# Optimization experiments

Hardware: AMD Instinct MI355X
Metric: run time of the kernel (lower is better)

The kernel has to match this reference:

```python
import jax, jax.numpy as jnp
from jax import lax
import numpy as np

B, CIN, COUT, H, W = 32, 64, 64, 128, 128
KH = KW = 1
STRIDE = (1, 1)
PADDING = ((0, 0), (0, 0))


def setup_inputs() -> dict:
    key = jax.random.key(0)
    k1, k2, k3, k4 = jax.random.split(key, 4)
    x_quant = jax.random.randint(k1, (B, CIN, H, W), 0, 256, dtype=jnp.int32)  # uint8 values
    weight_int8 = jax.random.randint(k2, (COUT, CIN, KH, KW), -127, 128, dtype=jnp.int32)
    weight_scale = jax.random.uniform(k3, (COUT, 1, 1, 1), dtype=jnp.float32, minval=0.001, maxval=0.02)
    weight_zero_point = jnp.zeros((COUT, 1, 1, 1), dtype=jnp.int32)
    bias_fp32 = jax.random.normal(k4, (COUT,), dtype=jnp.float32) * 0.1
    return {
        "x_quant": x_quant,
        "input_scale": jnp.float32(0.02),
        "input_zero_point": jnp.int32(128),
        "weight_int8": weight_int8,
        "weight_scale": weight_scale,
        "weight_zero_point": weight_zero_point,
        "bias_fp32": bias_fp32,
        "output_scale": jnp.float32(0.05),
        "output_zero_point": jnp.int32(128),
    }


def reference(x_quant, input_scale, input_zero_point, weight_int8, weight_scale,
              weight_zero_point, bias_fp32, output_scale, output_zero_point):
    # dequant (zero-point subtract) in fp32
    x = x_quant.astype(jnp.float32) - input_zero_point.astype(jnp.float32)          # [B,Cin,H,W]
    w = weight_int8.astype(jnp.float32) - weight_zero_point.astype(jnp.float32)     # [O,I,kh,kw]
    conv = lax.conv_general_dilated(
        x, w, window_strides=STRIDE, padding=PADDING,
        dimension_numbers=("NCHW", "OIHW", "NCHW"))                                 # [B,O,H',W']
    # requantize: per-out-channel scale + bias, round, clamp to uint8 range
    requant_scale = (input_scale * weight_scale / output_scale).reshape(1, COUT, 1, 1)
    bias_term = (bias_fp32 / output_scale).reshape(1, COUT, 1, 1)
    final_float = conv * requant_scale + bias_term
    requant = jnp.round(final_float) + output_zero_point.astype(jnp.float32)
    out_q = jnp.clip(requant, 0.0, 255.0).astype(jnp.uint8)
    return out_q
```

## Files before the change

### kernel.cpp

```cpp
#include <hip/hip_runtime.h>

#define CIN   64
#define COUT  64
#define HW    16384
#define NPIX  (32 * HW)

#define BLOCKS 512
#define SPAN   1024
#define GRP    128
#define NGRP   (SPAN / GRP)

__global__ void prep_kernel(const int* __restrict__ w,
                            const float* __restrict__ wscale,
                            const int* __restrict__ wzp,
                            const float* __restrict__ bias,
                            const float* __restrict__ is_p,
                            const int* __restrict__ izp_p,
                            const float* __restrict__ os_p,
                            const int* __restrict__ ozp_p,
                            int* __restrict__ wp,
                            float4* __restrict__ params) {
    int o = threadIdx.x;
    if (o >= COUT) return;
    int zp = wzp[o];
    int sum = 0;
    #pragma unroll
    for (int k = 0; k < 16; ++k) {
        int c0 = w[o * CIN + 4 * k + 0] - zp;
        int c1 = w[o * CIN + 4 * k + 1] - zp;
        int c2 = w[o * CIN + 4 * k + 2] - zp;
        int c3 = w[o * CIN + 4 * k + 3] - zp;
        sum += c0 + c1 + c2 + c3;
        wp[o * 16 + k] = (c0 & 0xff) | ((c1 & 0xff) << 8) |
                         ((c2 & 0xff) << 16) | ((c3 & 0xff) << 24);
    }
    float4 pr;
    pr.x = is_p[0] * wscale[o] / os_p[0];
    pr.y = bias[o] / os_p[0] + (float)ozp_p[0];
    pr.z = 0.0f;
    pr.w = __int_as_float((128 - izp_p[0]) * sum);
    params[o] = pr;
}

__global__ __launch_bounds__(256) void conv_kernel(
    const int* __restrict__ x,
    const int* __restrict__ wp_g,
    const float4* __restrict__ params_g,
    int* __restrict__ out) {

    __shared__ int s_x[2][CIN * GRP];

    const int tid  = threadIdx.x;
    const int lane = tid & 63;
    const int wv   = tid >> 6;
    const int px   = tid & (GRP - 1);
    const int oh   = __builtin_amdgcn_readfirstlane(tid >> 7);

    const int pix_base = blockIdx.x * SPAN;
    const int bimg = pix_base >> 14;
    const int p0   = pix_base & (HW - 1);
    const int* ximg = x   + bimg * (CIN * HW) + p0;
    int*       oimg = out + bimg * (COUT * HW) + p0;

    auto issue = [&](int g, int nb) {
        const int* gbase = ximg + g * GRP + ((lane & 31) * 4);
        #pragma unroll
        for (int j = 0; j < 8; ++j) {
            int c = wv * 16 + 2 * j + (lane >> 5);
            const int* gp = gbase + c * HW;
            int* lp = &s_x[nb][(wv * 16 + 2 * j) * GRP];
            __builtin_amdgcn_global_load_lds(
                (const __attribute__((address_space(1))) void*)gp,
                (__attribute__((address_space(3))) void*)lp, 16, 0, 0);
        }
    };

    issue(0, 0);

    for (int g = 0; g < NGRP; ++g) {
        __syncthreads();
        if (g + 1 < NGRP) issue(g + 1, (g + 1) & 1);

        const int* xp = &s_x[g & 1][px];
        int pk[16];
        #pragma unroll
        for (int cg = 0; cg < 16; ++cg) {
            int v0 = xp[(4 * cg + 0) * GRP];
            int v1 = xp[(4 * cg + 1) * GRP];
            int v2 = xp[(4 * cg + 2) * GRP];
            int v3 = xp[(4 * cg + 3) * GRP];
            pk[cg] = (v0 | (v1 << 8) | (v2 << 16) | (v3 << 24)) ^ 0x80808080;
        }

        int* og = oimg + g * GRP + px;
        #pragma unroll 4
        for (int i = 0; i < 32; ++i) {
            int o = oh * 32 + i;
            const int4* wvp = (const int4*)(wp_g + o * 16);
            int4 w0 = wvp[0], w1 = wvp[1], w2 = wvp[2], w3 = wvp[3];
            float4 pr = params_g[o];
            int acc = __float_as_int(pr.w);

            acc = __builtin_amdgcn_sdot4(pk[0],  w0.x, acc, false);
            acc = __builtin_amdgcn_sdot4(pk[1],  w0.y, acc, false);
            acc = __builtin_amdgcn_sdot4(pk[2],  w0.z, acc, false);
            acc = __builtin_amdgcn_sdot4(pk[3],  w0.w, acc, false);
            acc = __builtin_amdgcn_sdot4(pk[4],  w1.x, acc, false);
            acc = __builtin_amdgcn_sdot4(pk[5],  w1.y, acc, false);
            acc = __builtin_amdgcn_sdot4(pk[6],  w1.z, acc, false);
            acc = __builtin_amdgcn_sdot4(pk[7],  w1.w, acc, false);
            acc = __builtin_amdgcn_sdot4(pk[8],  w2.x, acc, false);
            acc = __builtin_amdgcn_sdot4(pk[9],  w2.y, acc, false);
            acc = __builtin_amdgcn_sdot4(pk[10], w2.z, acc, false);
            acc = __builtin_amdgcn_sdot4(pk[11], w2.w, acc, false);
            acc = __builtin_amdgcn_sdot4(pk[12], w3.x, acc, false);
            acc = __builtin_amdgcn_sdot4(pk[13], w3.y, acc, false);
            acc = __builtin_amdgcn_sdot4(pk[14], w3.z, acc, false);
            acc = __builtin_amdgcn_sdot4(pk[15], w3.w, acc, false);

            float f = fmaf((float)acc, pr.x, pr.y);
            f = rintf(f);
            f = fminf(fmaxf(f, 0.0f), 255.0f);
            __builtin_nontemporal_store((int)f, og + o * HW);
        }
    }
}

extern "C" void kernel_launch(void* const* d_in, const int* in_sizes, int n_in,
                              void* d_out, int out_size, void* d_ws, size_t ws_size,
                              hipStream_t stream) {
    const int*   x      = (const int*)d_in[0];
    const float* is_p   = (const float*)d_in[1];
    const int*   izp_p  = (const int*)d_in[2];
    const int*   w      = (const int*)d_in[3];
    const float* wscale = (const float*)d_in[4];
    const int*   wzp    = (const int*)d_in[5];
    const float* bias   = (const float*)d_in[6];
    const float* os_p   = (const float*)d_in[7];
    const int*   ozp_p  = (const int*)d_in[8];

    int* out = (int*)d_out;

    int*    wp     = (int*)d_ws;
    float4* params = (float4*)((char*)d_ws + 4096);

    prep_kernel<<<1, 64, 0, stream>>>(w, wscale, wzp, bias, is_p, izp_p, os_p,
                                      ozp_p, wp, params);

    conv_kernel<<<BLOCKS, 256, 0, stream>>>(x, wp, params, out);
}
```

Measured before the change: 276.8 us.

## Replace LDS double-buffered staging with direct per-thread global loads over all outputs

Removes the shared-memory staging via global_load_lds and its barrier-synchronized double buffering. Each thread now loads its pixel's 64 input channels straight from global memory and computes all 64 output channels, handling two pixels spaced half the tensor apart. The grid becomes 2048 blocks of 128 threads. This drops LDS traffic and barriers and the split of output channels across half-blocks. In exchange it loses the asynchronous prefetch overlap and relies on enough waves in flight to hide global load latency.

```diff
diff --git a/kernel.cpp b/kernel.cpp
--- a/kernel.cpp
+++ b/kernel.cpp
@@ -4,11 +4,7 @@
 #define COUT  64
 #define HW    16384
 #define NPIX  (32 * HW)
-
-#define BLOCKS 512
-#define SPAN   1024
-#define GRP    128
-#define NGRP   (SPAN / GRP)
+#define HALF  (NPIX / 2)
 
 __global__ void prep_kernel(const int* __restrict__ w,
                             const float* __restrict__ wscale,
@@ -42,62 +38,43 @@
     params[o] = pr;
 }
 
-__global__ __launch_bounds__(256) void conv_kernel(
+__device__ __forceinline__ int pack4(int v0, int v1, int v2, int v3) {
+    return (v0 | (v1 << 8) | (v2 << 16) | (v3 << 24)) ^ 0x80808080;
+}
+
+__global__ __launch_bounds__(128) void conv_kernel(
     const int* __restrict__ x,
     const int* __restrict__ wp_g,
     const float4* __restrict__ params_g,
     int* __restrict__ out) {
 
-    __shared__ int s_x[2][CIN * GRP];
+    const int tid = threadIdx.x;
+    const int t0  = blockIdx.x * 128 + tid;
 
-    const int tid  = threadIdx.x;
-    const int lane = tid & 63;
-    const int wv   = tid >> 6;
-    const int px   = tid & (GRP - 1);
-    const int oh   = __builtin_amdgcn_readfirstlane(tid >> 7);
+    #pragma unroll
+    for (int half = 0; half < 2; ++half) {
+        int t = t0 + half * HALF;
+        int b = t >> 14;
+        int p = t & (HW - 1);
 
-    const int pix_base = blockIdx.x * SPAN;
-    const int bimg = pix_base >> 14;
-    const int p0   = pix_base & (HW - 1);
-    const int* ximg = x   + bimg * (CIN * HW) + p0;
-    int*       oimg = out + bimg * (COUT * HW) + p0;
+        const int* xb = x + b * (CIN * HW) + p;
 
-    auto issue = [&](int g, int nb) {
-        const int* gbase = ximg + g * GRP + ((lane & 31) * 4);
-        #pragma unroll
-        for (int j = 0; j < 8; ++j) {
-            int c = wv * 16 + 2 * j + (lane >> 5);
-            const int* gp = gbase + c * HW;
-            int* lp = &s_x[nb][(wv * 16 + 2 * j) * GRP];
-            __builtin_amdgcn_global_load_lds(
-                (const __attribute__((address_space(1))) void*)gp,
-                (__attribute__((address_space(3))) void*)lp, 16, 0, 0);
-        }
-    };
-
-    issue(0, 0);
-
-    for (int g = 0; g < NGRP; ++g) {
-        __syncthreads();
-        if (g + 1 < NGRP) issue(g + 1, (g + 1) & 1);
-
-        const int* xp = &s_x[g & 1][px];
         int pk[16];
         #pragma unroll
         for (int cg = 0; cg < 16; ++cg) {
-            int v0 = xp[(4 * cg + 0) * GRP];
-            int v1 = xp[(4 * cg + 1) * GRP];
-            int v2 = xp[(4 * cg + 2) * GRP];
-            int v3 = xp[(4 * cg + 3) * GRP];
-            pk[cg] = (v0 | (v1 << 8) | (v2 << 16) | (v3 << 24)) ^ 0x80808080;
+            int v0 = xb[(4 * cg + 0) * HW];
+            int v1 = xb[(4 * cg + 1) * HW];
+            int v2 = xb[(4 * cg + 2) * HW];
+            int v3 = xb[(4 * cg + 3) * HW];
+            pk[cg] = pack4(v0, v1, v2, v3);
         }
 
-        int* og = oimg + g * GRP + px;
-        #pragma unroll 4
-        for (int i = 0; i < 32; ++i) {
-            int o = oh * 32 + i;
-            const int4* wvp = (const int4*)(wp_g + o * 16);
-            int4 w0 = wvp[0], w1 = wvp[1], w2 = wvp[2], w3 = wvp[3];
+        int* ob = out + b * (COUT * HW) + p;
+
+        #pragma unroll 8
+        for (int o = 0; o < COUT; ++o) {
+            const int4* wv = (const int4*)(wp_g + o * 16);
+            int4 w0 = wv[0], w1 = wv[1], w2 = wv[2], w3 = wv[3];
             float4 pr = params_g[o];
             int acc = __float_as_int(pr.w);
 
@@ -121,7 +98,7 @@
             float f = fmaf((float)acc, pr.x, pr.y);
             f = rintf(f);
             f = fminf(fmaxf(f, 0.0f), 255.0f);
-            __builtin_nontemporal_store((int)f, og + o * HW);
+            __builtin_nontemporal_store((int)f, ob + o * HW);
         }
     }
 }
@@ -147,5 +124,5 @@
     prep_kernel<<<1, 64, 0, stream>>>(w, wscale, wzp, bias, is_p, izp_p, os_p,
                                       ozp_p, wp, params);
 
-    conv_kernel<<<BLOCKS, 256, 0, stream>>>(x, wp, params, out);
+    conv_kernel<<<2048, 128, 0, stream>>>(x, wp, params, out);
 }
```

Measured after the change: 258.1 us. 6.7% less time.
